# Kernel tuning notes

Hardware: AMD Instinct MI355X
Metric: run time of the kernel (lower is better)

Reference implementation:

```python
import jax, jax.numpy as jnp
import numpy as np


def setup_inputs() -> dict:
    key = jax.random.key(0)
    ks = jax.random.split(key, 9)
    B, C, H, W = 16, 64, 64, 64
    s = 0.02
    return {
        "x": jax.random.normal(ks[0], (B, C, H, W), dtype=jnp.float32),
        "qw": jax.random.normal(ks[1], (C, C), dtype=jnp.float32) * s,
        "qb": jax.random.normal(ks[2], (C,), dtype=jnp.float32) * s,
        "kw": jax.random.normal(ks[3], (C, C), dtype=jnp.float32) * s,
        "kb": jax.random.normal(ks[4], (C,), dtype=jnp.float32) * s,
        "vw": jax.random.normal(ks[5], (C, C), dtype=jnp.float32) * s,
        "vb": jax.random.normal(ks[6], (C,), dtype=jnp.float32) * s,
        "ow": jax.random.normal(ks[7], (C, C), dtype=jnp.float32) * s,
        "ob": jax.random.normal(ks[8], (C,), dtype=jnp.float32) * s,
    }


def reference(x, qw, qb, kw, kb, vw, vb, ow, ob):
    # x: [B, C, H, W]; 1x1 convs == per-pixel linear maps with weight [out_ch, in_ch]
    B, C, H, W = x.shape
    S = H * W
    xt = x.reshape(B, C, S).transpose(0, 2, 1)  # [B, S, C] tokens over spatial positions
    Q = jnp.einsum("bsc,oc->bso", xt, qw) + qb
    K = jnp.einsum("bsc,oc->bso", xt, kw) + kb
    V = jnp.einsum("bsc,oc->bso", xt, vw) + vb
    scale = 1.0 / jnp.sqrt(jnp.asarray(C, dtype=x.dtype))
    scores = jnp.einsum("bqc,bkc->bqk", Q, K) * scale  # [B, S, S]
    attn = jax.nn.softmax(scores, axis=-1)
    out = jnp.einsum("bqk,bkc->bqc", attn, V)  # [B, S, C]
    out = jnp.einsum("bsc,oc->bso", out, ow) + ob  # out 1x1 conv
    return out.transpose(0, 2, 1).reshape(B, C, H, W)
```

## Files before the change

kernel.cpp:

```cpp
#include <hip/hip_runtime.h>
#include <stdint.h>

#define SS 4096
#define CC 64
#define BB 16

typedef unsigned short u16;
typedef __attribute__((ext_vector_type(8))) __bf16 bf16x8;
typedef __attribute__((ext_vector_type(8))) short short8;
typedef __attribute__((ext_vector_type(4))) float f32x4;

__device__ __forceinline__ uint32_t pkbf(float a, float b) {
    uint32_t ua = __float_as_uint(a) + 0x8000u;
    uint32_t ub = __float_as_uint(b) + 0x8000u;
    return __builtin_amdgcn_perm(ub, ua, 0x07060302u);
}

__global__ __launch_bounds__(256) void qkv_kernel(
    const float* __restrict__ x,
    const float* __restrict__ qw, const float* __restrict__ qb,
    const float* __restrict__ kw, const float* __restrict__ kb,
    const float* __restrict__ vw, const float* __restrict__ vb,
    u16* __restrict__ Q, u16* __restrict__ K, u16* __restrict__ VT)
{
    const int b    = blockIdx.x >> 5;
    const int s0   = (blockIdx.x & 31) << 7;
    const int tid  = threadIdx.x;
    const int w    = tid >> 6;
    const int lane = tid & 63;
    const int lq   = lane & 15;
    const int quad = lane >> 4;

    __shared__ u16 xt[128 * 72];
    __shared__ u16 wt[3][64 * 72];
    __shared__ u16 bounce[4][16 * 72];

    for (int m = 0; m < 3; ++m) {
        const float* wsrc = (m == 0) ? qw : ((m == 1) ? kw : vw);
#pragma unroll
        for (int i = 0; i < 8; ++i) {
            int p  = tid + (i << 8);
            int o  = p >> 5;
            int cp = p & 31;
            const float* wp = wsrc + o * 64 + cp * 2;
            ((uint32_t*)&wt[m][o * 72])[cp] = pkbf(wp[0], wp[1]);
        }
    }
    {
        const int sl = tid & 127;
        const int g  = tid >> 7;
        const float* xp = x + (size_t)b * CC * SS + s0 + sl;
#pragma unroll
        for (int i = 0; i < 16; ++i) {
            int p = g + (i << 1);
            float f0 = xp[(size_t)(2 * p) * SS];
            float f1 = xp[(size_t)(2 * p + 1) * SS];
            ((uint32_t*)&xt[sl * 72])[p] = pkbf(f0, f1);
        }
    }
    __syncthreads();

    const float QSCALE = 0.125f * 1.44269504088896340736f;

    for (int m = 0; m < 3; ++m) {
        const float* bsrc = (m == 0) ? qb : ((m == 1) ? kb : vb);
        bf16x8 bfr[2][4];
#pragma unroll
        for (int kk = 0; kk < 2; ++kk)
#pragma unroll
            for (int nt = 0; nt < 4; ++nt)
                bfr[kk][nt] = *(const bf16x8*)&wt[m][(nt * 16 + lq) * 72 + kk * 32 + quad * 8];

        float bias[4];
#pragma unroll
        for (int nt = 0; nt < 4; ++nt) bias[nt] = bsrc[nt * 16 + lq];

#pragma unroll
        for (int mt = 0; mt < 2; ++mt) {
            const int srow = w * 32 + mt * 16;
            bf16x8 a0 = *(const bf16x8*)&xt[(srow + lq) * 72 + quad * 8];
            bf16x8 a1 = *(const bf16x8*)&xt[(srow + lq) * 72 + 32 + quad * 8];

            f32x4 acc[4];
#pragma unroll
            for (int nt = 0; nt < 4; ++nt)
                acc[nt] = (f32x4){bias[nt], bias[nt], bias[nt], bias[nt]};
#pragma unroll
            for (int nt = 0; nt < 4; ++nt) {
                acc[nt] = __builtin_amdgcn_mfma_f32_16x16x32_bf16(a0, bfr[0][nt], acc[nt], 0, 0, 0);
                acc[nt] = __builtin_amdgcn_mfma_f32_16x16x32_bf16(a1, bfr[1][nt], acc[nt], 0, 0, 0);
            }

            if (m == 2) {
#pragma unroll
                for (int nt = 0; nt < 4; ++nt) {
                    int c = nt * 16 + lq;
                    uint32_t p0 = pkbf(acc[nt][0], acc[nt][1]);
                    uint32_t p1 = pkbf(acc[nt][2], acc[nt][3]);
                    u16* dst = VT + ((size_t)(b * CC + c)) * SS + s0 + srow + quad * 4;
                    uint2 pv; pv.x = p0; pv.y = p1;
                    *(uint2*)dst = pv;
                }
            } else {
                const float scl = (m == 0) ? QSCALE : 1.0f;
                u16* bb = bounce[w];
#pragma unroll
                for (int nt = 0; nt < 4; ++nt)
#pragma unroll
                    for (int r = 0; r < 4; ++r)
                        bb[(quad * 4 + r) * 72 + nt * 16 + lq] =
                            (u16)((__float_as_uint(acc[nt][r] * scl) + 0x8000u) >> 16);

                const int row = lane >> 2;
                const int ch  = (lane & 3) << 4;
                short8 v0 = *(const short8*)&bb[row * 72 + ch];
                short8 v1 = *(const short8*)&bb[row * 72 + ch + 8];
                u16* dst = ((m == 0) ? Q : K) + ((size_t)(b * SS + s0 + srow + row)) * CC + ch;
                *(short8*)dst = v0;
                *(short8*)(dst + 8) = v1;
            }
        }
    }
}

__global__ __launch_bounds__(256, 4) void flash_kernel(
    const u16* __restrict__ Q, const u16* __restrict__ K,
    const u16* __restrict__ Vt, u16* __restrict__ AO)
{
    const int b    = blockIdx.x >> 6;
    const int q0   = (blockIdx.x & 63) << 6;
    const int tid  = threadIdx.x;
    const int w    = tid >> 6;
    const int lane = tid & 63;
    const int lq   = lane & 15;
    const int quad = lane >> 4;

    __shared__ u16 lds_k[2][64 * 64];
    __shared__ u16 lds_v[2][64 * 64];
    __shared__ u16 lds_p[4][16 * 64];

    const u16* qbase = Q + ((size_t)(b * SS + q0 + w * 16 + lq)) * CC + quad * 8;
    bf16x8 qf0 = *(const bf16x8*)(qbase);
    bf16x8 qf1 = *(const bf16x8*)(qbase + 32);

    f32x4 ot[4];
#pragma unroll
    for (int ct = 0; ct < 4; ++ct) ot[ct] = (f32x4){0.f, 0.f, 0.f, 0.f};
    float lp0 = 0.f, lp1 = 0.f, lp2 = 0.f, lp3 = 0.f;

    const int srow = tid >> 2;
    const int a    = tid & 3;
    const u16* kg = K + ((size_t)(b * SS + srow)) * CC + a * 16;
    const u16* vg = Vt + ((size_t)(b * CC + srow)) * SS + a * 16;
    const int sw0 = srow * 64 + (((a << 1)    ) ^ (srow & 7)) * 8;
    const int sw1 = srow * 64 + (((a << 1) | 1) ^ (srow & 7)) * 8;

    {
        short8 k0 = *(const short8*)(kg);
        short8 k1 = *(const short8*)(kg + 8);
        short8 v0 = *(const short8*)(vg);
        short8 v1 = *(const short8*)(vg + 8);
        *(short8*)&lds_k[0][sw0] = k0;
        *(short8*)&lds_k[0][sw1] = k1;
        *(short8*)&lds_v[0][sw0] = v0;
        *(short8*)&lds_v[0][sw1] = v1;
    }

    const int lsw = lq & 7;
    u16* pw = lds_p[w];

    for (int kt = 0; kt < 64; ++kt) {
        __syncthreads();
        const int buf = kt & 1;

        const int ktn = (kt + 1) & 63;
        const u16* kgn = kg + (size_t)ktn * (64 * CC);
        const u16* vgn = vg + ktn * 64;
        short8 nk0 = *(const short8*)(kgn);
        short8 nk1 = *(const short8*)(kgn + 8);
        short8 nv0 = *(const short8*)(vgn);
        short8 nv1 = *(const short8*)(vgn + 8);

        f32x4 sa[4];
#pragma unroll
        for (int mt = 0; mt < 4; ++mt) sa[mt] = (f32x4){0.f, 0.f, 0.f, 0.f};
#pragma unroll
        for (int kc = 0; kc < 2; ++kc) {
            bf16x8 qf = kc ? qf1 : qf0;
#pragma unroll
            for (int mt = 0; mt < 4; ++mt) {
                bf16x8 kf = *(const bf16x8*)
                    &lds_k[buf][(mt * 16 + lq) * 64 + (((kc << 2) + quad) ^ lsw) * 8];
                sa[mt] = __builtin_amdgcn_mfma_f32_16x16x32_bf16(kf, qf, sa[mt], 0, 0, 0);
            }
        }

#pragma unroll
        for (int mt = 0; mt < 4; ++mt) {
            float p0 = __builtin_amdgcn_exp2f(sa[mt][0]);
            float p1 = __builtin_amdgcn_exp2f(sa[mt][1]);
            float p2 = __builtin_amdgcn_exp2f(sa[mt][2]);
            float p3 = __builtin_amdgcn_exp2f(sa[mt][3]);
            lp0 += p0; lp1 += p1; lp2 += p2; lp3 += p3;
            uint2 pv;
            pv.x = pkbf(p0, p1);
            pv.y = pkbf(p2, p3);
            *(uint2*)&pw[lq * 64 + (((mt << 1) + (quad >> 1)) ^ lsw) * 8 + (quad & 1) * 4] = pv;
        }

#pragma unroll
        for (int kc = 0; kc < 2; ++kc) {
            bf16x8 pf = *(const bf16x8*)&pw[lq * 64 + (((kc << 2) + quad) ^ lsw) * 8];
#pragma unroll
            for (int ct = 0; ct < 4; ++ct) {
                bf16x8 vf = *(const bf16x8*)
                    &lds_v[buf][(ct * 16 + lq) * 64 + (((kc << 2) + quad) ^ lsw) * 8];
                ot[ct] = __builtin_amdgcn_mfma_f32_16x16x32_bf16(vf, pf, ot[ct], 0, 0, 0);
            }
        }

        u16* lkd = lds_k[buf ^ 1];
        u16* lvd = lds_v[buf ^ 1];
        *(short8*)&lkd[sw0] = nk0;
        *(short8*)&lkd[sw1] = nk1;
        *(short8*)&lvd[sw0] = nv0;
        *(short8*)&lvd[sw1] = nv1;
    }

    float l = (lp0 + lp1) + (lp2 + lp3);
    l += __shfl_xor(l, 16);
    l += __shfl_xor(l, 32);
    const float inv = 1.0f / l;

    u16* obase = AO + ((size_t)(b * SS + q0 + w * 16 + lq)) * CC;
#pragma unroll
    for (int ct = 0; ct < 4; ++ct) {
        uint2 pv;
        pv.x = pkbf(ot[ct][0] * inv, ot[ct][1] * inv);
        pv.y = pkbf(ot[ct][2] * inv, ot[ct][3] * inv);
        *(uint2*)(obase + ct * 16 + quad * 4) = pv;
    }
}

__global__ __launch_bounds__(256) void out_kernel(
    const u16* __restrict__ AO, const float* __restrict__ ow,
    const float* __restrict__ ob, float* __restrict__ out)
{
    const int b    = blockIdx.x >> 5;
    const int s0   = (blockIdx.x & 31) << 7;
    const int tid  = threadIdx.x;
    const int w    = tid >> 6;
    const int lane = tid & 63;
    const int lq   = lane & 15;
    const int quad = lane >> 4;

    __shared__ u16 wt[64 * 72];

#pragma unroll
    for (int i = 0; i < 8; ++i) {
        int p  = tid + (i << 8);
        int o  = p >> 5;
        int cp = p & 31;
        const float* wp = ow + o * 64 + cp * 2;
        ((uint32_t*)&wt[o * 72])[cp] = pkbf(wp[0], wp[1]);
    }
    __syncthreads();

    bf16x8 bfr[2][4];
#pragma unroll
    for (int kk = 0; kk < 2; ++kk)
#pragma unroll
        for (int nt = 0; nt < 4; ++nt)
            bfr[kk][nt] = *(const bf16x8*)&wt[(nt * 16 + lq) * 72 + kk * 32 + quad * 8];

    float bias[4];
#pragma unroll
    for (int nt = 0; nt < 4; ++nt) bias[nt] = ob[nt * 16 + lq];

#pragma unroll
    for (int mt = 0; mt < 2; ++mt) {
        const int srow = w * 32 + mt * 16;
        const u16* ap = AO + ((size_t)(b * SS + s0 + srow + lq)) * CC + quad * 8;
        bf16x8 a0 = *(const bf16x8*)(ap);
        bf16x8 a1 = *(const bf16x8*)(ap + 32);

        f32x4 acc[4];
#pragma unroll
        for (int nt = 0; nt < 4; ++nt)
            acc[nt] = (f32x4){bias[nt], bias[nt], bias[nt], bias[nt]};
#pragma unroll
        for (int nt = 0; nt < 4; ++nt) {
            acc[nt] = __builtin_amdgcn_mfma_f32_16x16x32_bf16(a0, bfr[0][nt], acc[nt], 0, 0, 0);
            acc[nt] = __builtin_amdgcn_mfma_f32_16x16x32_bf16(a1, bfr[1][nt], acc[nt], 0, 0, 0);
        }

#pragma unroll
        for (int nt = 0; nt < 4; ++nt) {
            int o = nt * 16 + lq;
            float* dst = out + ((size_t)(b * CC + o)) * SS + s0 + srow + quad * 4;
            *(f32x4*)dst = acc[nt];
        }
    }
}

extern "C" void kernel_launch(void* const* d_in, const int* in_sizes, int n_in,
                              void* d_out, int out_size, void* d_ws, size_t ws_size,
                              hipStream_t stream)
{
    const float* x  = (const float*)d_in[0];
    const float* qw = (const float*)d_in[1];
    const float* qb = (const float*)d_in[2];
    const float* kw = (const float*)d_in[3];
    const float* kb = (const float*)d_in[4];
    const float* vw = (const float*)d_in[5];
    const float* vb = (const float*)d_in[6];
    const float* ow = (const float*)d_in[7];
    const float* ob = (const float*)d_in[8];
    float* out = (float*)d_out;

    const size_t T = (size_t)BB * SS * CC;
    u16* Q  = (u16*)d_ws;
    u16* K  = Q + T;
    u16* VT = K + T;
    u16* AO = VT + T;

    qkv_kernel<<<dim3(BB * 32), dim3(256), 0, stream>>>(x, qw, qb, kw, kb, vw, vb, Q, K, VT);
    flash_kernel<<<dim3(BB * 64), dim3(256), 0, stream>>>(Q, K, VT, AO);
    out_kernel<<<dim3(BB * 32), dim3(256), 0, stream>>>(AO, ow, ob, out);
}
```

Measured before the change: 193.3 us.

## Fuse output projection into flash kernel, pre-convert weights, double query rows per block

Adds a small kernel that converts all four weight matrices to bf16 once, so the QKV and output stages read prepacked weights instead of converting them per block. The QKV kernel now uses 64-row tiles with more blocks. The flash kernel handles 128 queries per block as two 64-query groups, so each K/V tile loaded into LDS is reused twice, and launch bounds are lowered to 2 blocks per CU. The output 1x1 conv is fused into the flash epilogue, which removes the AO round trip and the third kernel. In exchange the flash kernel uses more registers and occupancy drops, and launching half as many flash blocks may underfill the GPU.

```diff
diff --git a/kernel.cpp b/kernel.cpp
--- a/kernel.cpp
+++ b/kernel.cpp
@@ -16,43 +16,41 @@
     return __builtin_amdgcn_perm(ub, ua, 0x07060302u);
 }
 
-__global__ __launch_bounds__(256) void qkv_kernel(
-    const float* __restrict__ x,
-    const float* __restrict__ qw, const float* __restrict__ qb,
-    const float* __restrict__ kw, const float* __restrict__ kb,
-    const float* __restrict__ vw, const float* __restrict__ vb,
+__global__ void wpre_kernel(const float* __restrict__ qw, const float* __restrict__ kw,
+                            const float* __restrict__ vw, const float* __restrict__ ow,
+                            u16* __restrict__ wsb)
+{
+    int idx = blockIdx.x * 256 + threadIdx.x;
+    const float* src = (idx < 2048) ? qw : (idx < 4096) ? kw
+                     : (idx < 6144) ? vw : ow;
+    int pair = idx & 2047;
+    ((uint32_t*)wsb)[idx] = pkbf(src[pair * 2], src[pair * 2 + 1]);
+}
+
+__global__ __launch_bounds__(256, 4) void qkv_kernel(
+    const float* __restrict__ x, const u16* __restrict__ wsb,
+    const float* __restrict__ qb, const float* __restrict__ kb,
+    const float* __restrict__ vb,
     u16* __restrict__ Q, u16* __restrict__ K, u16* __restrict__ VT)
 {
-    const int b    = blockIdx.x >> 5;
-    const int s0   = (blockIdx.x & 31) << 7;
+    const int b    = blockIdx.x & 15;
+    const int s0   = (blockIdx.x >> 4) << 6;
     const int tid  = threadIdx.x;
     const int w    = tid >> 6;
     const int lane = tid & 63;
     const int lq   = lane & 15;
     const int quad = lane >> 4;
 
-    __shared__ u16 xt[128 * 72];
-    __shared__ u16 wt[3][64 * 72];
+    __shared__ u16 xt[64 * 72];
     __shared__ u16 bounce[4][16 * 72];
 
-    for (int m = 0; m < 3; ++m) {
-        const float* wsrc = (m == 0) ? qw : ((m == 1) ? kw : vw);
+    {
+        const int sl = tid & 63;
+        const int g  = tid >> 6;
+        const float* xp = x + (size_t)b * CC * SS + s0 + sl;
 #pragma unroll
         for (int i = 0; i < 8; ++i) {
-            int p  = tid + (i << 8);
-            int o  = p >> 5;
-            int cp = p & 31;
-            const float* wp = wsrc + o * 64 + cp * 2;
-            ((uint32_t*)&wt[m][o * 72])[cp] = pkbf(wp[0], wp[1]);
-        }
-    }
-    {
-        const int sl = tid & 127;
-        const int g  = tid >> 7;
-        const float* xp = x + (size_t)b * CC * SS + s0 + sl;
-#pragma unroll
-        for (int i = 0; i < 16; ++i) {
-            int p = g + (i << 1);
+            int p = g + (i << 2);
             float f0 = xp[(size_t)(2 * p) * SS];
             float f1 = xp[(size_t)(2 * p + 1) * SS];
             ((uint32_t*)&xt[sl * 72])[p] = pkbf(f0, f1);
@@ -60,75 +58,70 @@
     }
     __syncthreads();
 
+    bf16x8 a0 = *(const bf16x8*)&xt[(w * 16 + lq) * 72 + quad * 8];
+    bf16x8 a1 = *(const bf16x8*)&xt[(w * 16 + lq) * 72 + 32 + quad * 8];
+
     const float QSCALE = 0.125f * 1.44269504088896340736f;
 
     for (int m = 0; m < 3; ++m) {
         const float* bsrc = (m == 0) ? qb : ((m == 1) ? kb : vb);
+        const u16* wm = wsb + m * 4096;
         bf16x8 bfr[2][4];
 #pragma unroll
-        for (int kk = 0; kk < 2; ++kk)
+        for (int kc = 0; kc < 2; ++kc)
 #pragma unroll
             for (int nt = 0; nt < 4; ++nt)
-                bfr[kk][nt] = *(const bf16x8*)&wt[m][(nt * 16 + lq) * 72 + kk * 32 + quad * 8];
-
-        float bias[4];
-#pragma unroll
-        for (int nt = 0; nt < 4; ++nt) bias[nt] = bsrc[nt * 16 + lq];
-
-#pragma unroll
-        for (int mt = 0; mt < 2; ++mt) {
-            const int srow = w * 32 + mt * 16;
-            bf16x8 a0 = *(const bf16x8*)&xt[(srow + lq) * 72 + quad * 8];
-            bf16x8 a1 = *(const bf16x8*)&xt[(srow + lq) * 72 + 32 + quad * 8];
-
-            f32x4 acc[4];
+                bfr[kc][nt] = *(const bf16x8*)&wm[(nt * 16 + lq) * 64 + kc * 32 + quad * 8];
+
+        f32x4 acc[4];
+#pragma unroll
+        for (int nt = 0; nt < 4; ++nt) {
+            float bv = bsrc[nt * 16 + lq];
+            acc[nt] = (f32x4){bv, bv, bv, bv};
+        }
+#pragma unroll
+        for (int nt = 0; nt < 4; ++nt) {
+            acc[nt] = __builtin_amdgcn_mfma_f32_16x16x32_bf16(a0, bfr[0][nt], acc[nt], 0, 0, 0);
+            acc[nt] = __builtin_amdgcn_mfma_f32_16x16x32_bf16(a1, bfr[1][nt], acc[nt], 0, 0, 0);
+        }
+
+        if (m == 2) {
+#pragma unroll
+            for (int nt = 0; nt < 4; ++nt) {
+                int c = nt * 16 + lq;
+                uint2 pv;
+                pv.x = pkbf(acc[nt][0], acc[nt][1]);
+                pv.y = pkbf(acc[nt][2], acc[nt][3]);
+                *(uint2*)(VT + ((size_t)(b * CC + c)) * SS + s0 + w * 16 + quad * 4) = pv;
+            }
+        } else {
+            const float scl = (m == 0) ? QSCALE : 1.0f;
+            u16* bb = bounce[w];
 #pragma unroll
             for (int nt = 0; nt < 4; ++nt)
-                acc[nt] = (f32x4){bias[nt], bias[nt], bias[nt], bias[nt]};
-#pragma unroll
-            for (int nt = 0; nt < 4; ++nt) {
-                acc[nt] = __builtin_amdgcn_mfma_f32_16x16x32_bf16(a0, bfr[0][nt], acc[nt], 0, 0, 0);
-                acc[nt] = __builtin_amdgcn_mfma_f32_16x16x32_bf16(a1, bfr[1][nt], acc[nt], 0, 0, 0);
-            }
-
-            if (m == 2) {
-#pragma unroll
-                for (int nt = 0; nt < 4; ++nt) {
-                    int c = nt * 16 + lq;
-                    uint32_t p0 = pkbf(acc[nt][0], acc[nt][1]);
-                    uint32_t p1 = pkbf(acc[nt][2], acc[nt][3]);
-                    u16* dst = VT + ((size_t)(b * CC + c)) * SS + s0 + srow + quad * 4;
-                    uint2 pv; pv.x = p0; pv.y = p1;
-                    *(uint2*)dst = pv;
-                }
-            } else {
-                const float scl = (m == 0) ? QSCALE : 1.0f;
-                u16* bb = bounce[w];
-#pragma unroll
-                for (int nt = 0; nt < 4; ++nt)
-#pragma unroll
-                    for (int r = 0; r < 4; ++r)
-                        bb[(quad * 4 + r) * 72 + nt * 16 + lq] =
-                            (u16)((__float_as_uint(acc[nt][r] * scl) + 0x8000u) >> 16);
-
-                const int row = lane >> 2;
-                const int ch  = (lane & 3) << 4;
-                short8 v0 = *(const short8*)&bb[row * 72 + ch];
-                short8 v1 = *(const short8*)&bb[row * 72 + ch + 8];
-                u16* dst = ((m == 0) ? Q : K) + ((size_t)(b * SS + s0 + srow + row)) * CC + ch;
-                *(short8*)dst = v0;
-                *(short8*)(dst + 8) = v1;
-            }
-        }
-    }
-}
-
-__global__ __launch_bounds__(256, 4) void flash_kernel(
+#pragma unroll
+                for (int r = 0; r < 4; ++r)
+                    bb[(quad * 4 + r) * 72 + nt * 16 + lq] =
+                        (u16)((__float_as_uint(acc[nt][r] * scl) + 0x8000u) >> 16);
+
+            const int row = lane >> 2;
+            const int ch  = (lane & 3) << 4;
+            short8 v0 = *(const short8*)&bb[row * 72 + ch];
+            short8 v1 = *(const short8*)&bb[row * 72 + ch + 8];
+            u16* dst = ((m == 0) ? Q : K) + ((size_t)(b * SS + s0 + w * 16 + row)) * CC + ch;
+            *(short8*)dst = v0;
+            *(short8*)(dst + 8) = v1;
+        }
+    }
+}
+
+__global__ __launch_bounds__(256, 2) void flash_kernel(
     const u16* __restrict__ Q, const u16* __restrict__ K,
-    const u16* __restrict__ Vt, u16* __restrict__ AO)
+    const u16* __restrict__ Vt, const u16* __restrict__ owb,
+    const float* __restrict__ ob, float* __restrict__ out)
 {
-    const int b    = blockIdx.x >> 6;
-    const int q0   = (blockIdx.x & 63) << 6;
+    const int b    = blockIdx.x & 15;
+    const int q0   = (blockIdx.x >> 4) << 7;
     const int tid  = threadIdx.x;
     const int w    = tid >> 6;
     const int lane = tid & 63;
@@ -137,16 +130,22 @@
 
     __shared__ u16 lds_k[2][64 * 64];
     __shared__ u16 lds_v[2][64 * 64];
-    __shared__ u16 lds_p[4][16 * 64];
-
-    const u16* qbase = Q + ((size_t)(b * SS + q0 + w * 16 + lq)) * CC + quad * 8;
-    bf16x8 qf0 = *(const bf16x8*)(qbase);
-    bf16x8 qf1 = *(const bf16x8*)(qbase + 32);
-
-    f32x4 ot[4];
-#pragma unroll
-    for (int ct = 0; ct < 4; ++ct) ot[ct] = (f32x4){0.f, 0.f, 0.f, 0.f};
-    float lp0 = 0.f, lp1 = 0.f, lp2 = 0.f, lp3 = 0.f;
+    __shared__ u16 lds_p[8][16 * 72];
+
+    bf16x8 qf[2][2];
+#pragma unroll
+    for (int g = 0; g < 2; ++g) {
+        const u16* qp = Q + ((size_t)(b * SS + q0 + g * 64 + w * 16 + lq)) * CC + quad * 8;
+        qf[g][0] = *(const bf16x8*)(qp);
+        qf[g][1] = *(const bf16x8*)(qp + 32);
+    }
+
+    f32x4 ot[2][4];
+#pragma unroll
+    for (int g = 0; g < 2; ++g)
+#pragma unroll
+        for (int ct = 0; ct < 4; ++ct) ot[g][ct] = (f32x4){0.f, 0.f, 0.f, 0.f};
+    float lp[2][4] = {{0.f, 0.f, 0.f, 0.f}, {0.f, 0.f, 0.f, 0.f}};
 
     const int srow = tid >> 2;
     const int a    = tid & 3;
@@ -167,7 +166,8 @@
     }
 
     const int lsw = lq & 7;
-    u16* pw = lds_p[w];
+    u16* pw0 = lds_p[(w << 1)];
+    u16* pw1 = lds_p[(w << 1) | 1];
 
     for (int kt = 0; kt < 64; ++kt) {
         __syncthreads();
@@ -181,41 +181,63 @@
         short8 nv0 = *(const short8*)(vgn);
         short8 nv1 = *(const short8*)(vgn + 8);
 
-        f32x4 sa[4];
-#pragma unroll
-        for (int mt = 0; mt < 4; ++mt) sa[mt] = (f32x4){0.f, 0.f, 0.f, 0.f};
-#pragma unroll
-        for (int kc = 0; kc < 2; ++kc) {
-            bf16x8 qf = kc ? qf1 : qf0;
+        bf16x8 kf[2][4];
+#pragma unroll
+        for (int kc = 0; kc < 2; ++kc)
+#pragma unroll
+            for (int mt = 0; mt < 4; ++mt)
+                kf[kc][mt] = *(const bf16x8*)
+                    &lds_k[buf][(mt * 16 + lq) * 64 + (((kc << 2) + quad) ^ lsw) * 8];
+
+        f32x4 sa[2][4];
+#pragma unroll
+        for (int g = 0; g < 2; ++g)
+#pragma unroll
+            for (int mt = 0; mt < 4; ++mt) sa[g][mt] = (f32x4){0.f, 0.f, 0.f, 0.f};
+#pragma unroll
+        for (int g = 0; g < 2; ++g)
+#pragma unroll
+            for (int kc = 0; kc < 2; ++kc)
+#pragma unroll
+                for (int mt = 0; mt < 4; ++mt)
+                    sa[g][mt] = __builtin_amdgcn_mfma_f32_16x16x32_bf16(
+                        kf[kc][mt], qf[g][kc], sa[g][mt], 0, 0, 0);
+
+#pragma unroll
+        for (int g = 0; g < 2; ++g) {
+            u16* pw = g ? pw1 : pw0;
 #pragma unroll
             for (int mt = 0; mt < 4; ++mt) {
-                bf16x8 kf = *(const bf16x8*)
-                    &lds_k[buf][(mt * 16 + lq) * 64 + (((kc << 2) + quad) ^ lsw) * 8];
-                sa[mt] = __builtin_amdgcn_mfma_f32_16x16x32_bf16(kf, qf, sa[mt], 0, 0, 0);
+                float p0 = __builtin_amdgcn_exp2f(sa[g][mt][0]);
+                float p1 = __builtin_amdgcn_exp2f(sa[g][mt][1]);
+                float p2 = __builtin_amdgcn_exp2f(sa[g][mt][2]);
+                float p3 = __builtin_amdgcn_exp2f(sa[g][mt][3]);
+                lp[g][0] += p0; lp[g][1] += p1; lp[g][2] += p2; lp[g][3] += p3;
+                uint2 pv;
+                pv.x = pkbf(p0, p1);
+                pv.y = pkbf(p2, p3);
+                *(uint2*)&pw[lq * 72 + mt * 16 + quad * 4] = pv;
             }
         }
 
-#pragma unroll
-        for (int mt = 0; mt < 4; ++mt) {
-            float p0 = __builtin_amdgcn_exp2f(sa[mt][0]);
-            float p1 = __builtin_amdgcn_exp2f(sa[mt][1]);
-            float p2 = __builtin_amdgcn_exp2f(sa[mt][2]);
-            float p3 = __builtin_amdgcn_exp2f(sa[mt][3]);
-            lp0 += p0; lp1 += p1; lp2 += p2; lp3 += p3;
-            uint2 pv;
-            pv.x = pkbf(p0, p1);
-            pv.y = pkbf(p2, p3);
-            *(uint2*)&pw[lq * 64 + (((mt << 1) + (quad >> 1)) ^ lsw) * 8 + (quad & 1) * 4] = pv;
-        }
-
-#pragma unroll
-        for (int kc = 0; kc < 2; ++kc) {
-            bf16x8 pf = *(const bf16x8*)&pw[lq * 64 + (((kc << 2) + quad) ^ lsw) * 8];
-#pragma unroll
-            for (int ct = 0; ct < 4; ++ct) {
-                bf16x8 vf = *(const bf16x8*)
+        bf16x8 vf[2][4];
+#pragma unroll
+        for (int kc = 0; kc < 2; ++kc)
+#pragma unroll
+            for (int ct = 0; ct < 4; ++ct)
+                vf[kc][ct] = *(const bf16x8*)
                     &lds_v[buf][(ct * 16 + lq) * 64 + (((kc << 2) + quad) ^ lsw) * 8];
-                ot[ct] = __builtin_amdgcn_mfma_f32_16x16x32_bf16(vf, pf, ot[ct], 0, 0, 0);
+
+#pragma unroll
+        for (int g = 0; g < 2; ++g) {
+            const u16* pw = g ? pw1 : pw0;
+#pragma unroll
+            for (int kc = 0; kc < 2; ++kc) {
+                bf16x8 pf = *(const bf16x8*)&pw[lq * 72 + kc * 32 + quad * 8];
+#pragma unroll
+                for (int ct = 0; ct < 4; ++ct)
+                    ot[g][ct] = __builtin_amdgcn_mfma_f32_16x16x32_bf16(
+                        vf[kc][ct], pf, ot[g][ct], 0, 0, 0);
             }
         }
 
@@ -227,62 +249,33 @@
         *(short8*)&lvd[sw1] = nv1;
     }
 
-    float l = (lp0 + lp1) + (lp2 + lp3);
-    l += __shfl_xor(l, 16);
-    l += __shfl_xor(l, 32);
-    const float inv = 1.0f / l;
-
-    u16* obase = AO + ((size_t)(b * SS + q0 + w * 16 + lq)) * CC;
-#pragma unroll
-    for (int ct = 0; ct < 4; ++ct) {
-        uint2 pv;
-        pv.x = pkbf(ot[ct][0] * inv, ot[ct][1] * inv);
-        pv.y = pkbf(ot[ct][2] * inv, ot[ct][3] * inv);
-        *(uint2*)(obase + ct * 16 + quad * 4) = pv;
-    }
-}
-
-__global__ __launch_bounds__(256) void out_kernel(
-    const u16* __restrict__ AO, const float* __restrict__ ow,
-    const float* __restrict__ ob, float* __restrict__ out)
-{
-    const int b    = blockIdx.x >> 5;
-    const int s0   = (blockIdx.x & 31) << 7;
-    const int tid  = threadIdx.x;
-    const int w    = tid >> 6;
-    const int lane = tid & 63;
-    const int lq   = lane & 15;
-    const int quad = lane >> 4;
-
-    __shared__ u16 wt[64 * 72];
-
-#pragma unroll
-    for (int i = 0; i < 8; ++i) {
-        int p  = tid + (i << 8);
-        int o  = p >> 5;
-        int cp = p & 31;
-        const float* wp = ow + o * 64 + cp * 2;
-        ((uint32_t*)&wt[o * 72])[cp] = pkbf(wp[0], wp[1]);
-    }
-    __syncthreads();
-
-    bf16x8 bfr[2][4];
-#pragma unroll
-    for (int kk = 0; kk < 2; ++kk)
+    bf16x8 wf[2][4];
+#pragma unroll
+    for (int kc = 0; kc < 2; ++kc)
 #pragma unroll
         for (int nt = 0; nt < 4; ++nt)
-            bfr[kk][nt] = *(const bf16x8*)&wt[(nt * 16 + lq) * 72 + kk * 32 + quad * 8];
-
+            wf[kc][nt] = *(const bf16x8*)&owb[(nt * 16 + lq) * 64 + kc * 32 + quad * 8];
     float bias[4];
 #pragma unroll
     for (int nt = 0; nt < 4; ++nt) bias[nt] = ob[nt * 16 + lq];
 
 #pragma unroll
-    for (int mt = 0; mt < 2; ++mt) {
-        const int srow = w * 32 + mt * 16;
-        const u16* ap = AO + ((size_t)(b * SS + s0 + srow + lq)) * CC + quad * 8;
-        bf16x8 a0 = *(const bf16x8*)(ap);
-        bf16x8 a1 = *(const bf16x8*)(ap + 32);
+    for (int g = 0; g < 2; ++g) {
+        float l = (lp[g][0] + lp[g][1]) + (lp[g][2] + lp[g][3]);
+        l += __shfl_xor(l, 16);
+        l += __shfl_xor(l, 32);
+        const float inv = 1.0f / l;
+
+        u16* po = g ? pw1 : pw0;
+#pragma unroll
+        for (int ct = 0; ct < 4; ++ct) {
+            uint2 pv;
+            pv.x = pkbf(ot[g][ct][0] * inv, ot[g][ct][1] * inv);
+            pv.y = pkbf(ot[g][ct][2] * inv, ot[g][ct][3] * inv);
+            *(uint2*)&po[lq * 72 + ct * 16 + quad * 4] = pv;
+        }
+        bf16x8 oa0 = *(const bf16x8*)&po[lq * 72 + quad * 8];
+        bf16x8 oa1 = *(const bf16x8*)&po[lq * 72 + 32 + quad * 8];
 
         f32x4 acc[4];
 #pragma unroll
@@ -290,14 +283,13 @@
             acc[nt] = (f32x4){bias[nt], bias[nt], bias[nt], bias[nt]};
 #pragma unroll
         for (int nt = 0; nt < 4; ++nt) {
-            acc[nt] = __builtin_amdgcn_mfma_f32_16x16x32_bf16(a0, bfr[0][nt], acc[nt], 0, 0, 0);
-            acc[nt] = __builtin_amdgcn_mfma_f32_16x16x32_bf16(a1, bfr[1][nt], acc[nt], 0, 0, 0);
-        }
-
+            acc[nt] = __builtin_amdgcn_mfma_f32_16x16x32_bf16(oa0, wf[0][nt], acc[nt], 0, 0, 0);
+            acc[nt] = __builtin_amdgcn_mfma_f32_16x16x32_bf16(oa1, wf[1][nt], acc[nt], 0, 0, 0);
+        }
 #pragma unroll
         for (int nt = 0; nt < 4; ++nt) {
-            int o = nt * 16 + lq;
-            float* dst = out + ((size_t)(b * CC + o)) * SS + s0 + srow + quad * 4;
+            float* dst = out + ((size_t)(b * CC + nt * 16 + lq)) * SS
+                       + q0 + g * 64 + w * 16 + quad * 4;
             *(f32x4*)dst = acc[nt];
         }
     }
@@ -319,12 +311,12 @@
     float* out = (float*)d_out;
 
     const size_t T = (size_t)BB * SS * CC;
-    u16* Q  = (u16*)d_ws;
-    u16* K  = Q + T;
-    u16* VT = K + T;
-    u16* AO = VT + T;
-
-    qkv_kernel<<<dim3(BB * 32), dim3(256), 0, stream>>>(x, qw, qb, kw, kb, vw, vb, Q, K, VT);
-    flash_kernel<<<dim3(BB * 64), dim3(256), 0, stream>>>(Q, K, VT, AO);
-    out_kernel<<<dim3(BB * 32), dim3(256), 0, stream>>>(AO, ow, ob, out);
-}
+    u16* WSB = (u16*)d_ws;
+    u16* Q   = WSB + 4 * 4096;
+    u16* K   = Q + T;
+    u16* VT  = K + T;
+
+    wpre_kernel<<<dim3(32), dim3(256), 0, stream>>>(qw, kw, vw, ow, WSB);
+    qkv_kernel<<<dim3(BB * 64), dim3(256), 0, stream>>>(x, WSB, qb, kb, vb, Q, K, VT);
+    flash_kernel<<<dim3(BB * 32), dim3(256), 0, stream>>>(Q, K, VT, WSB + 3 * 4096, ob, out);
+}
```

Result: faster. 188.9 us (-2.3%).
